# Kernel optimization log

Hardware: AMD Instinct MI355X
Metric: run time of the kernel (lower is better)

## Reference

```python
import jax, jax.numpy as jnp
import numpy as np

B, C, H, W = 2, 128, 64, 64
EPS = 1e-5


def setup_inputs() -> dict:
    key = jax.random.key(0)
    ks = jax.random.split(key, 8)
    sc = 1.0 / np.sqrt(C)
    inp = {
        "x": jax.random.normal(ks[0], (B, C, H, W, 2), jnp.float32),
        # naive complex BN affine params: per-channel, per-component (real/imag)
        "bn_w": jnp.ones((C, 2), jnp.float32),
        "bn_b": jnp.zeros((C, 2), jnp.float32),
        # complex 1x1 conv weights: (out_c, in_c, 2) -> [..,0]=W_real, [..,1]=W_imag
        "wq": jax.random.normal(ks[1], (C, C, 2), jnp.float32) * sc,
        "bq": jnp.zeros((C, 2), jnp.float32),
        "wk": jax.random.normal(ks[2], (C, C, 2), jnp.float32) * sc,
        "bk": jnp.zeros((C, 2), jnp.float32),
        "wv": jax.random.normal(ks[3], (C, C, 2), jnp.float32) * sc,
        "bv": jnp.zeros((C, 2), jnp.float32),
        "gamma": jnp.float32(0.05),
    }
    return inp


def _complex_bn(x, w, b):
    # naive complex BN: normalize real and imag independently per channel
    # x: (B,C,H,W,2); stats over (B,H,W) per (C, component)
    mean = x.mean(axis=(0, 2, 3), keepdims=True)
    var = x.var(axis=(0, 2, 3), keepdims=True)
    xn = (x - mean) * jax.lax.rsqrt(var + EPS)
    return xn * w[None, :, None, None, :] + b[None, :, None, None, :]


def _complex_conv1x1(x, w, b):
    # x: (B,C,H,W,2); w: (O,C,2); b: (O,2)
    xr, xi = x[..., 0], x[..., 1]
    wr, wi = w[..., 0], w[..., 1]
    yr = jnp.einsum('oc,bchw->bohw', wr, xr) - jnp.einsum('oc,bchw->bohw', wi, xi)
    yi = jnp.einsum('oc,bchw->bohw', wr, xi) + jnp.einsum('oc,bchw->bohw', wi, xr)
    yr = yr + b[:, 0][None, :, None, None]
    yi = yi + b[:, 1][None, :, None, None]
    return jnp.stack([yr, yi], axis=-1)


def _attention(x, wq, bq, wk, bk, wv, bv, gamma):
    scale = C ** (-0.5)
    N = H * W
    # q,k,v: (B,C,H,W,2) -> (B,C,N,2) -> (B,N,C,2)
    to_tokens = lambda t: t.reshape(B, C, N, 2).transpose(0, 2, 1, 3)
    q = to_tokens(_complex_conv1x1(x, wq, bq))
    k = to_tokens(_complex_conv1x1(x, wk, bk))
    v = to_tokens(_complex_conv1x1(x, wv, bv))

    qr, qi = q[..., 0], q[..., 1]          # (B,N,C)
    kr, ki = k[..., 0], -k[..., 1]         # conjugate of k
    # k_t = conj(k) with token/channel axes swapped -> (B,C,N)
    ktr = kr.transpose(0, 2, 1)
    kti = ki.transpose(0, 2, 1)

    # complex matmul q @ k_t -> only the real part is used downstream
    attn_real = jnp.einsum('bnc,bcm->bnm', qr, ktr) - jnp.einsum('bnc,bcm->bnm', qi, kti)
    attn_w = jax.nn.softmax(attn_real * scale, axis=-1)  # (B,N,N)
    # dropout = identity (eval mode)

    # attn is purely real -> complex matmul reduces to two real matmuls
    out_r = jnp.einsum('bnm,bmc->bnc', attn_w, v[..., 0])
    out_i = jnp.einsum('bnm,bmc->bnc', attn_w, v[..., 1])
    out = jnp.stack([out_r, out_i], axis=-1)              # (B,N,C,2)
    out = out.transpose(0, 2, 1, 3).reshape(B, C, H, W, 2)
    return x + gamma * out


def reference(x, bn_w, bn_b, wq, bq, wk, bk, wv, bv, gamma):
    xn = _complex_bn(x, bn_w, bn_b)
    return _attention(xn, wq, bq, wk, bk, wv, bv, gamma)
```

## Files before the change

### kernel.cpp

```cpp
#include <hip/hip_runtime.h>
#include <hip/hip_bf16.h>
#include <hip/hip_fp8.h>

typedef __bf16 bf16_t;
typedef __bf16 bf16x8 __attribute__((ext_vector_type(8)));
typedef float  f32x4  __attribute__((ext_vector_type(4)));
typedef long   i64_t;

#define MFMA16(A,B,C) __builtin_amdgcn_mfma_f32_16x16x32_bf16((A),(B),(C),0,0,0)
#define MFMA8(A,B,C)  __builtin_amdgcn_mfma_f32_16x16x32_fp8_fp8((A),(B),(C),0,0,0)
#define MFMA85(A,B,C) __builtin_amdgcn_mfma_f32_16x16x32_bf8_fp8((A),(B),(C),0,0,0)

constexpr int Bn = 2, Cc = 128, Hh = 64, Wd = 64;
constexpr int N  = Hh * Wd;
constexpr int T  = Bn * N;
constexpr int D  = 2 * Cc;
constexpr int NSP = 4;
constexpr float EPS = 1e-5f;
constexpr float SCL = 0.08838834764831845f * 1.4426950408889634f;
constexpr float PSH = 9.0f;

__device__ __forceinline__ int tfrag(int row, int ch) {
    return (((ch >> 5) * 4 + (row >> 4)) << 10) +
           ((((ch >> 3) & 3) * 16 + (row & 15)) << 4) + (ch & 7) * 2;
}
__device__ __forceinline__ int tfrag8(int row, int ch) {
    return (((ch >> 5) * 4 + (row >> 4)) << 9) +
           ((((ch >> 3) & 3) * 16 + (row & 15)) << 3) + (ch & 7);
}
__device__ __forceinline__ int vfrag8(int ch, int key) {
    return (((key >> 5) * 16 + (ch >> 4)) << 9) +
           ((((key >> 3) & 3) * 16 + (ch & 15)) << 3) + (key & 7);
}

__device__ __forceinline__ unsigned char to_fp8(float v) {
    __hip_fp8_e4m3 t(v);
    return t.__x;
}
__device__ __forceinline__ unsigned char to_bf8(float v) {
    __hip_fp8_e5m2 t(v);
    return t.__x;
}

__device__ __forceinline__ void gl16(const void* g, void* l) {
    __builtin_amdgcn_global_load_lds(
        (const __attribute__((address_space(1))) void*)g,
        (__attribute__((address_space(3))) void*)l, 16, 0, 0);
}

__global__ void k_pre(const float* __restrict__ x, float4* __restrict__ part,
                      const float* __restrict__ wq, const float* __restrict__ wk,
                      const float* __restrict__ wv, const float* __restrict__ bq,
                      const float* __restrict__ bk, const float* __restrict__ bv,
                      char* __restrict__ Wg, float* __restrict__ bt) {
    int tid = threadIdx.x;
    if (blockIdx.x < 512) {
        int bid = blockIdx.x;
        int q = bid >> 7, c = bid & 127;
        float sr = 0.f, si = 0.f, qr = 0.f, qi = 0.f;
        for (int b = 0; b < Bn; ++b) {
            const float2* p = (const float2*)x + (size_t)(b * Cc + c) * N + q * 1024;
            for (int i = tid; i < 1024; i += 256) {
                float2 v = p[i];
                sr += v.x; si += v.y; qr += v.x * v.x; qi += v.y * v.y;
            }
        }
        #pragma unroll
        for (int d = 32; d >= 1; d >>= 1) {
            sr += __shfl_xor(sr, d); si += __shfl_xor(si, d);
            qr += __shfl_xor(qr, d); qi += __shfl_xor(qi, d);
        }
        __shared__ float red[4][4];
        int w = tid >> 6;
        if ((tid & 63) == 0) { red[w][0] = sr; red[w][1] = si; red[w][2] = qr; red[w][3] = qi; }
        __syncthreads();
        if (tid == 0) {
            part[c * 4 + q] = make_float4(red[0][0] + red[1][0] + red[2][0] + red[3][0],
                                          red[0][1] + red[1][1] + red[2][1] + red[3][1],
                                          red[0][2] + red[1][2] + red[2][2] + red[3][2],
                                          red[0][3] + red[1][3] + red[2][3] + red[3][3]);
        }
    } else {
        int o = blockIdx.x - 512;
        int k = tid;
        int proj = o >> 8, oc = o & 255;
        const float* wsrc = proj == 0 ? wq : (proj == 1 ? wk : wv);
        const float* bsrc = proj == 0 ? bq : (proj == 1 ? bk : bv);
        int co = oc >> 7, oo = oc & 127;
        int c = k & 127, kc = k >> 7;
        float val;
        if (co == 0) val = (kc == 0) ? wsrc[(oo * 128 + c) * 2 + 0] : -wsrc[(oo * 128 + c) * 2 + 1];
        else         val = (kc == 0) ? wsrc[(oo * 128 + c) * 2 + 1] :  wsrc[(oo * 128 + c) * 2 + 0];
        int tile = o >> 6, row = o & 63;
        *(bf16_t*)(Wg + (size_t)tile * 32768 + tfrag(row, k)) = (bf16_t)val;
        if (k == 0) bt[o] = bsrc[oo * 2 + co];
    }
}

__global__ void k_norm(const float* __restrict__ x, const float4* __restrict__ part,
                       const float* __restrict__ bn_w, const float* __restrict__ bn_b,
                       char* __restrict__ XNg) {
    __shared__ float4 ssl[128];
    __shared__ __align__(16) char Tsh[32768];
    int blk = blockIdx.x;
    int b = blk >> 6, hw0 = (blk & 63) * 64;
    int tid = threadIdx.x;
    if (tid < 128) {
        float4 p0 = part[tid * 4 + 0], p1 = part[tid * 4 + 1];
        float4 p2 = part[tid * 4 + 2], p3 = part[tid * 4 + 3];
        float sr = p0.x + p1.x + p2.x + p3.x, si = p0.y + p1.y + p2.y + p3.y;
        float qr = p0.z + p1.z + p2.z + p3.z, qi = p0.w + p1.w + p2.w + p3.w;
        const float inv = 1.0f / (float)(Bn * N);
        float mr = sr * inv, mi = si * inv;
        float vr = qr * inv - mr * mr, vi = qi * inv - mi * mi;
        float scr = bn_w[tid * 2 + 0] * rsqrtf(vr + EPS);
        float sci = bn_w[tid * 2 + 1] * rsqrtf(vi + EPS);
        ssl[tid] = make_float4(scr, bn_b[tid * 2 + 0] - mr * scr,
                               sci, bn_b[tid * 2 + 1] - mi * sci);
    }
    __syncthreads();
    const float2* xin = (const float2*)x;
    #pragma unroll
    for (int it = 0; it < 32; ++it) {
        int idx = it * 256 + tid;
        int c = idx >> 6, hw = idx & 63;
        size_t gi = (size_t)(b * Cc + c) * N + hw0 + hw;
        float2 v = xin[gi];
        float4 s = ssl[c];
        *(bf16_t*)(Tsh + tfrag(hw, c))       = (bf16_t)(v.x * s.x + s.y);
        *(bf16_t*)(Tsh + tfrag(hw, c + 128)) = (bf16_t)(v.y * s.z + s.w);
    }
    __syncthreads();
    #pragma unroll
    for (int it = 0; it < 8; ++it) {
        int idx = it * 256 + tid;
        *(uint4*)(XNg + (size_t)blk * 32768 + idx * 16) = *(const uint4*)(Tsh + idx * 16);
    }
}

__global__ __launch_bounds__(256) void k_qkv(const char* __restrict__ XNg,
        const char* __restrict__ Wg, const float* __restrict__ bt,
        char* __restrict__ Qg, char* __restrict__ Kg, char* __restrict__ Vg) {
    __shared__ __align__(16) char Xsh[32768];
    __shared__ __align__(16) char Wsh[32768];
    int mx = blockIdx.x, ny = blockIdx.y;
    int tid = threadIdx.x;
    int w = tid >> 6, lane = tid & 63, n15 = lane & 15, quad = lane >> 4;
    const char* xs = XNg + (size_t)mx * 32768;
    const char* wsp = Wg + (size_t)ny * 32768;
    #pragma unroll
    for (int i = 0; i < 8; ++i) {
        int off = (w * 8 + i) * 1024 + lane * 16;
        gl16(xs + off, Xsh + off);
        gl16(wsp + off, Wsh + off);
    }
    __syncthreads();
    f32x4 acc[4] = {};
    #pragma unroll
    for (int ks = 0; ks < 8; ++ks) {
        bf16x8 a = *(const bf16x8*)(Xsh + (ks * 4 + w) * 1024 + lane * 16);
        #pragma unroll
        for (int t = 0; t < 4; ++t) {
            bf16x8 bw = *(const bf16x8*)(Wsh + (ks * 4 + t) * 1024 + lane * 16);
            acc[t] = MFMA16(a, bw, acc[t]);
        }
    }
    int proj = ny >> 2;
    int jb = (ny & 3) * 64;
    #pragma unroll
    for (int t = 0; t < 4; ++t) {
        int j = jb + t * 16 + n15;
        float bias = bt[ny * 64 + t * 16 + n15];
        #pragma unroll
        for (int r = 0; r < 4; ++r) {
            int tk = mx * 64 + w * 16 + quad * 4 + r;
            unsigned char v8 = to_fp8(acc[t][r] + bias);
            int bb = tk >> 12, n = tk & (N - 1);
            if (proj == 0) {
                *(unsigned char*)(Qg + (size_t)(tk >> 6) * 16384 + tfrag8(tk & 63, j)) = v8;
            } else {
                size_t tb = (size_t)(bb * 64 + (n >> 6)) * 16384;
                if (proj == 1) *(unsigned char*)(Kg + tb + tfrag8(n & 63, j)) = v8;
                else           *(unsigned char*)(Vg + tb + vfrag8(j, n & 63)) = v8;
            }
        }
    }
}

__global__ __launch_bounds__(256) void k_attn(const char* __restrict__ Qg,
        const char* __restrict__ Kg, const char* __restrict__ Vg,
        bf16_t* __restrict__ Opb, float* __restrict__ Lp) {
    __shared__ __align__(16) char Ksh[16384];
    __shared__ __align__(16) char Vsh[16384];
    __shared__ __align__(16) char Psh[4096];
    int bid = blockIdx.x;
    int grp = bid & 7, qt = bid >> 3;
    int sp = grp & 3, b = grp >> 2;
    int tid = threadIdx.x;
    int w = tid >> 6, lane = tid & 63, n15 = lane & 15, quad = lane >> 4;
    int r = w >> 1, h = w & 1;

    const i64_t ONES = 0x3838383838383838L;

    i64_t qf[2][8];
    const char* qb = Qg + (size_t)(b * 64 + qt) * 16384;
    #pragma unroll
    for (int g = 0; g < 2; ++g)
        #pragma unroll
        for (int ks = 0; ks < 8; ++ks)
            qf[g][ks] = *(const i64_t*)(qb + ((ks * 4 + r * 2 + g) << 9) + lane * 8);

    f32x4 o[2][8] = {};
    f32x4 l_[2] = {};

    for (int kt = 0; kt < 16; ++kt) {
        size_t tb = (size_t)(b * 64 + sp * 16 + kt) * 16384;
        __syncthreads();
        #pragma unroll
        for (int i = 0; i < 4; ++i) {
            int off = (w * 4 + i) * 1024 + lane * 16;
            gl16(Kg + tb + off, Ksh + off);
            gl16(Vg + tb + off, Vsh + off);
        }
        __syncthreads();

        f32x4 s[2][2] = {};
        #pragma unroll
        for (int ks = 0; ks < 8; ++ks) {
            #pragma unroll
            for (int c = 0; c < 2; ++c) {
                i64_t kf = *(const i64_t*)(Ksh + ((ks * 4 + h * 2 + c) << 9) + lane * 8);
                s[0][c] = MFMA8(qf[0][ks], kf, s[0][c]);
                s[1][c] = MFMA8(qf[1][ks], kf, s[1][c]);
            }
        }
        #pragma unroll
        for (int g = 0; g < 2; ++g)
            #pragma unroll
            for (int c = 0; c < 2; ++c)
                #pragma unroll
                for (int ri = 0; ri < 4; ++ri) {
                    float p = __builtin_amdgcn_exp2f(s[g][c][ri] * SCL - PSH);
                    *(unsigned char*)(Psh + ((h * 4 + r * 2 + g) << 9) +
                        (((c * 2 + (n15 >> 3)) * 16 + quad * 4 + ri) << 3) +
                        (n15 & 7)) = to_bf8(p);
                }
        __syncthreads();

        #pragma unroll
        for (int k2 = 0; k2 < 2; ++k2) {
            i64_t pa0 = *(const i64_t*)(Psh + ((k2 * 4 + r * 2 + 0) << 9) + lane * 8);
            i64_t pa1 = *(const i64_t*)(Psh + ((k2 * 4 + r * 2 + 1) << 9) + lane * 8);
            l_[0] = MFMA85(pa0, ONES, l_[0]);
            l_[1] = MFMA85(pa1, ONES, l_[1]);
            #pragma unroll
            for (int ct = 0; ct < 8; ++ct) {
                i64_t vf = *(const i64_t*)(Vsh + ((k2 * 16 + h * 8 + ct) << 9) + lane * 8);
                o[0][ct] = MFMA85(pa0, vf, o[0][ct]);
                o[1][ct] = MFMA85(pa1, vf, o[1][ct]);
            }
        }
    }
    int tok0 = b * N + qt * 64 + r * 32;
    #pragma unroll
    for (int g = 0; g < 2; ++g) {
        #pragma unroll
        for (int ct = 0; ct < 8; ++ct)
            #pragma unroll
            for (int ri = 0; ri < 4; ++ri)
                Opb[((size_t)sp * T + tok0 + g * 16 + quad * 4 + ri) * D +
                    h * 128 + ct * 16 + n15] = (bf16_t)o[g][ct][ri];
        if (h == 0 && n15 == 0) {
            #pragma unroll
            for (int ri = 0; ri < 4; ++ri)
                Lp[sp * T + tok0 + g * 16 + quad * 4 + ri] = l_[g][ri];
        }
    }
}

__global__ void k_comb(const bf16_t* __restrict__ Opb, const float* __restrict__ Lp,
                       const float4* __restrict__ part, const float* __restrict__ bn_w,
                       const float* __restrict__ bn_b, const float* __restrict__ x,
                       const float* __restrict__ gamma, float* __restrict__ out) {
    __shared__ float4 ssl[128];
    __shared__ float wts[32];
    __shared__ float Ot[256 * 33];
    int blk = blockIdx.x;
    int b = blk >> 7, hw0 = (blk & 127) * 32;
    int tok0 = b * N + hw0;
    int tid = threadIdx.x;
    if (tid < 128) {
        float4 p0 = part[tid * 4 + 0], p1 = part[tid * 4 + 1];
        float4 p2 = part[tid * 4 + 2], p3 = part[tid * 4 + 3];
        float sr = p0.x + p1.x + p2.x + p3.x, si = p0.y + p1.y + p2.y + p3.y;
        float qr = p0.z + p1.z + p2.z + p3.z, qi = p0.w + p1.w + p2.w + p3.w;
        const float inv = 1.0f / (float)(Bn * N);
        float mr = sr * inv, mi = si * inv;
        float vr = qr * inv - mr * mr, vi = qi * inv - mi * mi;
        float scr = bn_w[tid * 2 + 0] * rsqrtf(vr + EPS);
        float sci = bn_w[tid * 2 + 1] * rsqrtf(vi + EPS);
        ssl[tid] = make_float4(scr, bn_b[tid * 2 + 0] - mr * scr,
                               sci, bn_b[tid * 2 + 1] - mi * sci);
    }
    if (tid < 32) {
        float Z = 0.f;
        #pragma unroll
        for (int s = 0; s < NSP; ++s) Z += Lp[s * T + tok0 + tid];
        wts[tid] = gamma[0] / Z;
    }
    __syncthreads();
    #pragma unroll
    for (int i = 0; i < 4; ++i) {
        int idx = i * 256 + tid;
        int tk = idx >> 5, chunk = idx & 31;
        size_t base = (size_t)(tok0 + tk) * D + chunk * 8;
        float acc[8] = {};
        #pragma unroll
        for (int s = 0; s < NSP; ++s) {
            bf16x8 v = *(const bf16x8*)(Opb + (size_t)s * T * D + base);
            #pragma unroll
            for (int j = 0; j < 8; ++j) acc[j] += (float)v[j];
        }
        float ww = wts[tk];
        #pragma unroll
        for (int j = 0; j < 8; ++j) Ot[(chunk * 8 + j) * 33 + tk] = acc[j] * ww;
    }
    __syncthreads();
    const float2* xin = (const float2*)x;
    float2* xo = (float2*)out;
    #pragma unroll
    for (int i = 0; i < 16; ++i) {
        int linear = i * 256 + tid;
        int c = linear >> 5, hwo = linear & 31;
        size_t idx = (size_t)(b * Cc + c) * N + hw0 + hwo;
        float2 v = xin[idx];
        float4 s = ssl[c];
        float2 res;
        res.x = v.x * s.x + s.y + Ot[c * 33 + hwo];
        res.y = v.y * s.z + s.w + Ot[(128 + c) * 33 + hwo];
        xo[idx] = res;
    }
}

extern "C" void kernel_launch(void* const* d_in, const int* in_sizes, int n_in,
                              void* d_out, int out_size, void* d_ws, size_t ws_size,
                              hipStream_t stream) {
    const float* x    = (const float*)d_in[0];
    const float* bn_w = (const float*)d_in[1];
    const float* bn_b = (const float*)d_in[2];
    const float* wq   = (const float*)d_in[3];
    const float* bq   = (const float*)d_in[4];
    const float* wk   = (const float*)d_in[5];
    const float* bk   = (const float*)d_in[6];
    const float* wv   = (const float*)d_in[7];
    const float* bv   = (const float*)d_in[8];
    const float* gam  = (const float*)d_in[9];
    float* out = (float*)d_out;

    char* ws = (char*)d_ws;
    size_t off = 0;
    auto alloc = [&](size_t bytes) -> void* {
        void* p = ws + off;
        off += (bytes + 255) & ~(size_t)255;
        return p;
    };
    float4* part = (float4*)alloc(512 * sizeof(float4));
    char*   XNg  = (char*)alloc((size_t)128 * 32768);
    char*   Wg   = (char*)alloc((size_t)12 * 32768);
    float*  bt   = (float*)alloc(768 * 4);
    char*   Qg   = (char*)alloc((size_t)128 * 16384);
    char*   Kg   = (char*)alloc((size_t)128 * 16384);
    char*   Vg   = (char*)alloc((size_t)128 * 16384);
    bf16_t* Opb  = (bf16_t*)alloc((size_t)NSP * T * D * 2);
    float*  Lp   = (float*)alloc((size_t)NSP * T * 4);

    k_pre<<<1280, 256, 0, stream>>>(x, part, wq, wk, wv, bq, bk, bv, Wg, bt);
    k_norm<<<128, 256, 0, stream>>>(x, part, bn_w, bn_b, XNg);
    k_qkv<<<dim3(128, 12), 256, 0, stream>>>(XNg, Wg, bt, Qg, Kg, Vg);
    k_attn<<<512, 256, 0, stream>>>(Qg, Kg, Vg, Opb, Lp);
    k_comb<<<256, 256, 0, stream>>>(Opb, Lp, part, bn_w, bn_b, x, gam, out);
}
```

Baseline: 147.1 us.

## Split attention keys eight ways and use packed hardware fp8 conversions

Doubles the key-split factor from four to eight, launching 1024 attention blocks that each process eight key tiles, and adds a launch-bounds occupancy hint. It also swaps the software fp8/bf8 conversion helpers for the packed cvt_pk_fp8/bf8 builtins in the QKV projection and the softmax probability writes. The extra split raises parallelism on the GPU's compute units but doubles the partial-output buffer and the combine work in k_comb. The occupancy hint may force register spills.

```diff
diff --git a/kernel.cpp b/kernel.cpp
--- a/kernel.cpp
+++ b/kernel.cpp
@@ -15,7 +15,7 @@
 constexpr int N  = Hh * Wd;
 constexpr int T  = Bn * N;
 constexpr int D  = 2 * Cc;
-constexpr int NSP = 4;
+constexpr int NSP = 8;
 constexpr float EPS = 1e-5f;
 constexpr float SCL = 0.08838834764831845f * 1.4426950408889634f;
 constexpr float PSH = 9.0f;
@@ -31,15 +31,6 @@
 __device__ __forceinline__ int vfrag8(int ch, int key) {
     return (((key >> 5) * 16 + (ch >> 4)) << 9) +
            ((((key >> 3) & 3) * 16 + (ch & 15)) << 3) + (key & 7);
-}
-
-__device__ __forceinline__ unsigned char to_fp8(float v) {
-    __hip_fp8_e4m3 t(v);
-    return t.__x;
-}
-__device__ __forceinline__ unsigned char to_bf8(float v) {
-    __hip_fp8_e5m2 t(v);
-    return t.__x;
 }
 
 __device__ __forceinline__ void gl16(const void* g, void* l) {
@@ -171,10 +162,15 @@
     for (int t = 0; t < 4; ++t) {
         int j = jb + t * 16 + n15;
         float bias = bt[ny * 64 + t * 16 + n15];
+        unsigned w01 = (unsigned)__builtin_amdgcn_cvt_pk_fp8_f32(
+            acc[t][0] + bias, acc[t][1] + bias, 0, false);
+        unsigned w23 = (unsigned)__builtin_amdgcn_cvt_pk_fp8_f32(
+            acc[t][2] + bias, acc[t][3] + bias, 0, false);
         #pragma unroll
         for (int r = 0; r < 4; ++r) {
             int tk = mx * 64 + w * 16 + quad * 4 + r;
-            unsigned char v8 = to_fp8(acc[t][r] + bias);
+            unsigned char v8 = (unsigned char)((r < 2 ? (w01 >> (8 * r))
+                                                      : (w23 >> (8 * (r - 2)))) & 0xff);
             int bb = tk >> 12, n = tk & (N - 1);
             if (proj == 0) {
                 *(unsigned char*)(Qg + (size_t)(tk >> 6) * 16384 + tfrag8(tk & 63, j)) = v8;
@@ -187,15 +183,15 @@
     }
 }
 
-__global__ __launch_bounds__(256) void k_attn(const char* __restrict__ Qg,
+__global__ __launch_bounds__(256, 4) void k_attn(const char* __restrict__ Qg,
         const char* __restrict__ Kg, const char* __restrict__ Vg,
         bf16_t* __restrict__ Opb, float* __restrict__ Lp) {
     __shared__ __align__(16) char Ksh[16384];
     __shared__ __align__(16) char Vsh[16384];
     __shared__ __align__(16) char Psh[4096];
     int bid = blockIdx.x;
-    int grp = bid & 7, qt = bid >> 3;
-    int sp = grp & 3, b = grp >> 2;
+    int grp = bid & 15, qt = bid >> 4;
+    int sp = grp & 7, b = grp >> 3;
     int tid = threadIdx.x;
     int w = tid >> 6, lane = tid & 63, n15 = lane & 15, quad = lane >> 4;
     int r = w >> 1, h = w & 1;
@@ -213,8 +209,8 @@
     f32x4 o[2][8] = {};
     f32x4 l_[2] = {};
 
-    for (int kt = 0; kt < 16; ++kt) {
-        size_t tb = (size_t)(b * 64 + sp * 16 + kt) * 16384;
+    for (int kt = 0; kt < 8; ++kt) {
+        size_t tb = (size_t)(b * 64 + sp * 8 + kt) * 16384;
         __syncthreads();
         #pragma unroll
         for (int i = 0; i < 4; ++i) {
@@ -237,14 +233,20 @@
         #pragma unroll
         for (int g = 0; g < 2; ++g)
             #pragma unroll
-            for (int c = 0; c < 2; ++c)
-                #pragma unroll
-                for (int ri = 0; ri < 4; ++ri) {
-                    float p = __builtin_amdgcn_exp2f(s[g][c][ri] * SCL - PSH);
-                    *(unsigned char*)(Psh + ((h * 4 + r * 2 + g) << 9) +
-                        (((c * 2 + (n15 >> 3)) * 16 + quad * 4 + ri) << 3) +
-                        (n15 & 7)) = to_bf8(p);
-                }
+            for (int c = 0; c < 2; ++c) {
+                float p0 = __builtin_amdgcn_exp2f(s[g][c][0] * SCL - PSH);
+                float p1 = __builtin_amdgcn_exp2f(s[g][c][1] * SCL - PSH);
+                float p2 = __builtin_amdgcn_exp2f(s[g][c][2] * SCL - PSH);
+                float p3 = __builtin_amdgcn_exp2f(s[g][c][3] * SCL - PSH);
+                unsigned w01 = (unsigned)__builtin_amdgcn_cvt_pk_bf8_f32(p0, p1, 0, false);
+                unsigned w23 = (unsigned)__builtin_amdgcn_cvt_pk_bf8_f32(p2, p3, 0, false);
+                char* pb = Psh + ((h * 4 + r * 2 + g) << 9) +
+                           (((c * 2 + (n15 >> 3)) * 16 + quad * 4) << 3) + (n15 & 7);
+                pb[0]  = (unsigned char)(w01 & 0xff);
+                pb[8]  = (unsigned char)((w01 >> 8) & 0xff);
+                pb[16] = (unsigned char)(w23 & 0xff);
+                pb[24] = (unsigned char)((w23 >> 8) & 0xff);
+            }
         __syncthreads();
 
         #pragma unroll
@@ -377,6 +379,6 @@
     k_pre<<<1280, 256, 0, stream>>>(x, part, wq, wk, wv, bq, bk, bv, Wg, bt);
     k_norm<<<128, 256, 0, stream>>>(x, part, bn_w, bn_b, XNg);
     k_qkv<<<dim3(128, 12), 256, 0, stream>>>(XNg, Wg, bt, Qg, Kg, Vg);
-    k_attn<<<512, 256, 0, stream>>>(Qg, Kg, Vg, Opb, Lp);
+    k_attn<<<1024, 256, 0, stream>>>(Qg, Kg, Vg, Opb, Lp);
     k_comb<<<256, 256, 0, stream>>>(Opb, Lp, part, bn_w, bn_b, x, gam, out);
 }
```

Measured after the change: 149.7 us. No clear change (+1.8%).
